# Optimization experiments

Measured on AMD Instinct MI355X. Metric: run time of the kernel, lower is better.

## Reference

```python
import jax, jax.numpy as jnp
import numpy as np

B, T, E, H, QKV = 4, 2048, 1024, 16, 64
D = E // H  # head_dim = 64


def setup_inputs() -> dict:
    key = jax.random.key(0)
    k1, k2, k3, k4 = jax.random.split(key, 4)
    scale = 1.0 / np.sqrt(D)
    x = jax.random.normal(k1, (B, T, E), dtype=jnp.float32)
    W_q = jax.random.normal(k2, (QKV, D), dtype=jnp.float32) * scale
    W_k = jax.random.normal(k3, (QKV, D), dtype=jnp.float32) * scale
    W_v = jax.random.normal(k4, (QKV, D), dtype=jnp.float32) * scale
    return {"x": x, "W_q": W_q, "W_k": W_k, "W_v": W_v}


def reference(x, W_q, W_k, W_v):
    Bx, Tx, Ex = x.shape
    d = Ex // H
    # [B,T,E] -> [B,H,T,D]  (same as torch view + permute(0,2,1,3))
    xh = x.reshape(Bx, Tx, H, d).transpose(0, 2, 1, 3)
    # Shared per-head projections: Linear(d -> qkv_dim), weight stored [out,in]
    Q = jnp.einsum("bhtd,qd->bhtq", xh, W_q)
    K = jnp.einsum("bhtd,qd->bhtq", xh, W_k)
    V = jnp.einsum("bhtd,qd->bhtq", xh, W_v)
    # NOTE: original scales by head_dim**0.5, not qkv_dim**0.5
    scores = jnp.einsum("bhtq,bhsq->bhts", Q, K) / jnp.asarray(d, x.dtype) ** 0.5
    attn = jax.nn.softmax(scores, axis=-1)
    out = jnp.einsum("bhts,bhsq->bhtq", attn, V) + V  # attention + V residual
    # per-head concat on last dim == head-major merge: [B,H,T,Q] -> [B,T,H*Q]
    return out.transpose(0, 2, 1, 3).reshape(Bx, Tx, H * W_q.shape[0])
```

## Files before the change

### kernel.cpp

```cpp
#include <hip/hip_runtime.h>

#define T_SEQ 2048
#define N_B   4
#define N_H   16
#define D_H   64
#define EMB   1024
#define CSC   0.18033688011f

typedef __attribute__((ext_vector_type(8))) short vshort8;
typedef __attribute__((ext_vector_type(4))) float vfloat4;

__device__ __forceinline__ ushort f2bf(float f) {
  union { float f; unsigned u; } v; v.f = f;
  unsigned u = v.u;
  return (ushort)((u + 0x7fffu + ((u >> 16) & 1u)) >> 16);
}
__device__ __forceinline__ unsigned pk2bf(float a, float b) {
  return (unsigned)f2bf(a) | ((unsigned)f2bf(b) << 16);
}
__device__ __forceinline__ float bf2f(ushort b) {
  union { unsigned u; float f; } v; v.u = ((unsigned)b) << 16;
  return v.f;
}
__device__ __forceinline__ float fexp2(float x) {
#if __has_builtin(__builtin_amdgcn_exp2f)
  return __builtin_amdgcn_exp2f(x);
#else
  return exp2f(x);
#endif
}
__device__ __forceinline__ unsigned permhi(float hi, float lo) {
  union { float f; unsigned u; } a, b; a.f = hi; b.f = lo;
#if __has_builtin(__builtin_amdgcn_perm)
  return __builtin_amdgcn_perm(a.u, b.u, 0x07060302u);
#else
  return (a.u & 0xFFFF0000u) | (b.u >> 16);
#endif
}


__global__ __launch_bounds__(256, 2) void proj_qkv(
    const float* __restrict__ x, const float* __restrict__ Wq,
    const float* __restrict__ Wk, const float* __restrict__ Wv,
    uint2* __restrict__ Qb, uint2* __restrict__ Kb, uint2* __restrict__ Vb) {
  const int wid  = threadIdx.x >> 6;
  const int lane = threadIdx.x & 63;
  const int l15  = lane & 15;
  const int quad = lane >> 4;
  const int gw = blockIdx.x * 4 + wid;
  const int rg = gw >> 4;
  const int h  = gw & 15;
  const int r0 = rg * 64;
  const int b  = r0 >> 11;
  const int bh = b * N_H + h;
  const int ts0 = (r0 & (T_SEQ - 1)) >> 4;

  vshort8 afr[4][2];
#pragma unroll
  for (int st = 0; st < 4; ++st) {
    const float* xp = x + (size_t)(r0 + st * 16 + l15) * EMB + h * D_H + quad * 8;
#pragma unroll
    for (int kc = 0; kc < 2; ++kc) {
      float4 a0 = *(const float4*)(xp + kc * 32);
      float4 a1 = *(const float4*)(xp + kc * 32 + 4);
      vshort8 t;
      t[0] = (short)f2bf(a0.x); t[1] = (short)f2bf(a0.y);
      t[2] = (short)f2bf(a0.z); t[3] = (short)f2bf(a0.w);
      t[4] = (short)f2bf(a1.x); t[5] = (short)f2bf(a1.y);
      t[6] = (short)f2bf(a1.z); t[7] = (short)f2bf(a1.w);
      afr[st][kc] = t;
    }
  }

  const float* Ws[3] = {Wq, Wk, Wv};
  uint2*       Bs[3] = {Qb, Kb, Vb};
#pragma unroll
  for (int m = 0; m < 3; ++m) {
    vshort8 wf[2][4];
#pragma unroll
    for (int kc = 0; kc < 2; ++kc)
#pragma unroll
      for (int nt = 0; nt < 4; ++nt) {
        const float* wp = Ws[m] + (nt * 16 + l15) * D_H + kc * 32 + quad * 8;
        float4 w0 = *(const float4*)(wp);
        float4 w1 = *(const float4*)(wp + 4);
        vshort8 t;
        t[0] = (short)f2bf(w0.x); t[1] = (short)f2bf(w0.y);
        t[2] = (short)f2bf(w0.z); t[3] = (short)f2bf(w0.w);
        t[4] = (short)f2bf(w1.x); t[5] = (short)f2bf(w1.y);
        t[6] = (short)f2bf(w1.z); t[7] = (short)f2bf(w1.w);
        wf[kc][nt] = t;
      }
    vfloat4 acc[4][4];
#pragma unroll
    for (int st = 0; st < 4; ++st)
#pragma unroll
      for (int nt = 0; nt < 4; ++nt) acc[st][nt] = (vfloat4){0.f, 0.f, 0.f, 0.f};
#pragma unroll
    for (int st = 0; st < 4; ++st)
#pragma unroll
      for (int kc = 0; kc < 2; ++kc)
#pragma unroll
        for (int nt = 0; nt < 4; ++nt)
          acc[st][nt] = (m < 2)
            ? __builtin_amdgcn_mfma_f32_16x16x32_bf16(wf[kc][nt], afr[st][kc], acc[st][nt], 0, 0, 0)
            : __builtin_amdgcn_mfma_f32_16x16x32_bf16(afr[st][kc], wf[kc][nt], acc[st][nt], 0, 0, 0);
    uint2* B = Bs[m];
#pragma unroll
    for (int st = 0; st < 4; ++st)
#pragma unroll
      for (int nt = 0; nt < 4; ++nt) {
        vfloat4 a = acc[st][nt];
        if (m == 0) { a[0] *= CSC; a[1] *= CSC; a[2] *= CSC; a[3] *= CSC; }
        uint2 w;
        w.x = pk2bf(a[0], a[1]);
        w.y = pk2bf(a[2], a[3]);
        B[(((size_t)bh * 128 + ts0 + st) * 4 + nt) * 64 + l15 * 4 + quad] = w;
      }
  }
}

__global__ __launch_bounds__(256, 2) void attn_fused(
    const uint2* __restrict__ Qb, const uint2* __restrict__ Kb,
    const uint2* __restrict__ Vb, float* __restrict__ out) {
  __shared__ ushort Pa[4 * 1024];

  const int tid  = threadIdx.x;
  const int wid  = tid >> 6;
  const int lane = tid & 63;
  const int l15  = lane & 15;
  const int quad = lane >> 4;
  const int qh   = quad >> 1;
  const int q1   = quad & 1;

  const int blk  = blockIdx.x;
  const int work = (blk & 7) * 64 + (blk >> 3);
  const int bh   = work >> 3;
  const int tblk = work & 7;
  const int b = bh >> 4, h = bh & 15;
  const int tstrip0 = tblk * 16 + wid * 4;

  const size_t hb = (size_t)bh * 128;
  const int laneoff = l15 * 4 + 2 * q1;

  vshort8 qf[4][2];
#pragma unroll
  for (int st = 0; st < 4; ++st)
#pragma unroll
    for (int kc = 0; kc < 2; ++kc)
      qf[st][kc] = *(const vshort8*)(&Qb[((hb + tstrip0 + st) * 4 + 2 * kc + qh) * 64 + laneoff]);

  vfloat4 oacc[4][4];
  float lsum[4];
#pragma unroll
  for (int st = 0; st < 4; ++st) {
#pragma unroll
    for (int nt = 0; nt < 4; ++nt) oacc[st][nt] = (vfloat4){0.f, 0.f, 0.f, 0.f};
    lsum[st] = 0.f;
  }

  ushort* Paw = &Pa[wid * 1024];
  const int parow = l15 * 64;
  const int swz   = l15 & 7;

  for (int ss = 0; ss < 128; ss += 4) {
    vshort8 kf[4][2];
#pragma unroll
    for (int snt = 0; snt < 4; ++snt)
#pragma unroll
      for (int kc = 0; kc < 2; ++kc)
        kf[snt][kc] = *(const vshort8*)(&Kb[((hb + ss + snt) * 4 + 2 * kc + qh) * 64 + laneoff]);
    vshort8 vf[2][4];
#pragma unroll
    for (int kc2 = 0; kc2 < 2; ++kc2)
#pragma unroll
      for (int dnt = 0; dnt < 4; ++dnt)
        vf[kc2][dnt] = *(const vshort8*)(&Vb[((hb + ss + 2 * kc2 + qh) * 4 + dnt) * 64 + laneoff]);

#pragma unroll
    for (int st = 0; st < 4; ++st) {
      vfloat4 sacc[4];
#pragma unroll
      for (int nt = 0; nt < 4; ++nt) sacc[nt] = (vfloat4){0.f, 0.f, 0.f, 0.f};
#pragma unroll
      for (int kc = 0; kc < 2; ++kc)
#pragma unroll
        for (int nt = 0; nt < 4; ++nt)
          sacc[nt] = __builtin_amdgcn_mfma_f32_16x16x32_bf16(kf[nt][kc], qf[st][kc], sacc[nt], 0, 0, 0);

      float ls = 0.f;
#pragma unroll
      for (int nt = 0; nt < 4; ++nt) {
        const float p0 = fexp2(sacc[nt][0]);
        const float p1 = fexp2(sacc[nt][1]);
        const float p2 = fexp2(sacc[nt][2]);
        const float p3 = fexp2(sacc[nt][3]);
        ls += (p0 + p1) + (p2 + p3);
        uint2 w;
        w.x = permhi(p1, p0);
        w.y = permhi(p3, p2);
        *(uint2*)(&Paw[parow + (((2 * nt + qh) ^ swz) << 3) + 4 * q1]) = w;
      }
      lsum[st] += ls;

#pragma unroll
      for (int kc2 = 0; kc2 < 2; ++kc2) {
        vshort8 pf = *(const vshort8*)(&Paw[parow + (((4 * kc2 + quad) ^ swz) << 3)]);
#pragma unroll
        for (int dnt = 0; dnt < 4; ++dnt)
          oacc[st][dnt] = __builtin_amdgcn_mfma_f32_16x16x32_bf16(pf, vf[kc2][dnt], oacc[st][dnt], 0, 0, 0);
      }
    }
  }

#pragma unroll
  for (int st = 0; st < 4; ++st) {
    float l = lsum[st];
    l += __shfl_xor(l, 16, 64);
    l += __shfl_xor(l, 32, 64);
    const float inv = 1.0f / l;
    float iT[4];
#pragma unroll
    for (int r = 0; r < 4; ++r) iT[r] = __shfl(inv, quad * 4 + r, 64);
    const int tstrip = tstrip0 + st;
#pragma unroll
    for (int nt = 0; nt < 4; ++nt) {
      uint2 vr = Vb[((hb + tstrip) * 4 + nt) * 64 + l15 * 4 + quad];
      float vres[4];
      vres[0] = bf2f((ushort)(vr.x & 0xFFFFu));
      vres[1] = bf2f((ushort)(vr.x >> 16));
      vres[2] = bf2f((ushort)(vr.y & 0xFFFFu));
      vres[3] = bf2f((ushort)(vr.y >> 16));
#pragma unroll
      for (int r = 0; r < 4; ++r) {
        const int t = tstrip * 16 + quad * 4 + r;
        out[((size_t)(b * T_SEQ + t)) * EMB + h * D_H + nt * 16 + l15] =
            oacc[st][nt][r] * iT[r] + vres[r];
      }
    }
  }
}

extern "C" void kernel_launch(void* const* d_in, const int* in_sizes, int n_in,
                              void* d_out, int out_size, void* d_ws, size_t ws_size,
                              hipStream_t stream) {
  const float* x  = (const float*)d_in[0];
  const float* Wq = (const float*)d_in[1];
  const float* Wk = (const float*)d_in[2];
  const float* Wv = (const float*)d_in[3];
  float* out = (float*)d_out;

  const size_t per = (size_t)64 * 128 * 4 * 16 * 4;
  uint2* Qb = (uint2*)d_ws;
  uint2* Kb = Qb + per;
  uint2* Vb = Kb + per;

  proj_qkv<<<512, 256, 0, stream>>>(x, Wq, Wk, Wv, Qb, Kb, Vb);
  attn_fused<<<512, 256, 0, stream>>>(Qb, Kb, Vb, out);
}
```

Measured before the change: 173.0 us.

## Pre-convert weights, shrink projection tiles, double-buffer K loads in attention

Adds a tiny kernel that converts the three weight matrices to bf16 MFMA fragment layout once, so the projection kernel no longer reconverts them per wave. The projection kernel now handles one 16-row strip per wave with 2048 blocks and a higher occupancy bound, trading per-wave reuse for more parallelism. The attention loop is restructured to prefetch the next K tile into a second register buffer while computing the current one, using precomputed base pointers. This raises register pressure and adds an extra kernel launch plus workspace use.

```diff
diff --git a/kernel.cpp b/kernel.cpp
--- a/kernel.cpp
+++ b/kernel.cpp
@@ -37,86 +37,86 @@
   return (a.u & 0xFFFF0000u) | (b.u >> 16);
 #endif
 }
-
-
-__global__ __launch_bounds__(256, 2) void proj_qkv(
-    const float* __restrict__ x, const float* __restrict__ Wq,
-    const float* __restrict__ Wk, const float* __restrict__ Wv,
+__device__ __forceinline__ vshort8 cvt8(const float* p) {
+  float4 w0 = *(const float4*)(p);
+  float4 w1 = *(const float4*)(p + 4);
+  vshort8 t;
+  t[0] = (short)f2bf(w0.x); t[1] = (short)f2bf(w0.y);
+  t[2] = (short)f2bf(w0.z); t[3] = (short)f2bf(w0.w);
+  t[4] = (short)f2bf(w1.x); t[5] = (short)f2bf(w1.y);
+  t[6] = (short)f2bf(w1.z); t[7] = (short)f2bf(w1.w);
+  return t;
+}
+
+
+__global__ void wconv(const float* __restrict__ Wq, const float* __restrict__ Wk,
+                      const float* __restrict__ Wv, ushort* __restrict__ Wb) {
+  const int lane = threadIdx.x & 63;
+  const int l15  = lane & 15;
+  const int quad = lane >> 4;
+  const float* Ws[3] = {Wq, Wk, Wv};
+#pragma unroll
+  for (int m = 0; m < 3; ++m)
+#pragma unroll
+    for (int kc = 0; kc < 2; ++kc)
+#pragma unroll
+      for (int nt = 0; nt < 4; ++nt) {
+        vshort8 t = cvt8(Ws[m] + (nt * 16 + l15) * D_H + kc * 32 + quad * 8);
+        *(vshort8*)(&Wb[(((m * 2 + kc) * 4 + nt) * 64 + lane) * 8]) = t;
+      }
+}
+
+__global__ __launch_bounds__(256, 4) void proj_qkv(
+    const float* __restrict__ x, const ushort* __restrict__ Wb,
     uint2* __restrict__ Qb, uint2* __restrict__ Kb, uint2* __restrict__ Vb) {
   const int wid  = threadIdx.x >> 6;
   const int lane = threadIdx.x & 63;
   const int l15  = lane & 15;
   const int quad = lane >> 4;
-  const int gw = blockIdx.x * 4 + wid;
-  const int rg = gw >> 4;
-  const int h  = gw & 15;
-  const int r0 = rg * 64;
-  const int b  = r0 >> 11;
-  const int bh = b * N_H + h;
-  const int ts0 = (r0 & (T_SEQ - 1)) >> 4;
-
-  vshort8 afr[4][2];
-#pragma unroll
-  for (int st = 0; st < 4; ++st) {
-    const float* xp = x + (size_t)(r0 + st * 16 + l15) * EMB + h * D_H + quad * 8;
-#pragma unroll
-    for (int kc = 0; kc < 2; ++kc) {
-      float4 a0 = *(const float4*)(xp + kc * 32);
-      float4 a1 = *(const float4*)(xp + kc * 32 + 4);
-      vshort8 t;
-      t[0] = (short)f2bf(a0.x); t[1] = (short)f2bf(a0.y);
-      t[2] = (short)f2bf(a0.z); t[3] = (short)f2bf(a0.w);
-      t[4] = (short)f2bf(a1.x); t[5] = (short)f2bf(a1.y);
-      t[6] = (short)f2bf(a1.z); t[7] = (short)f2bf(a1.w);
-      afr[st][kc] = t;
-    }
-  }
-
-  const float* Ws[3] = {Wq, Wk, Wv};
-  uint2*       Bs[3] = {Qb, Kb, Vb};
+  const int gw    = blockIdx.x * 4 + wid;
+  const int strip = gw >> 4;
+  const int h     = gw & 15;
+  const int r0    = strip * 16;
+  const int b     = r0 >> 11;
+  const int bh    = b * N_H + h;
+  const int ts    = (r0 & (T_SEQ - 1)) >> 4;
+
+  vshort8 afr[2];
+  {
+    const float* xp = x + (size_t)(r0 + l15) * EMB + h * D_H + quad * 8;
+    afr[0] = cvt8(xp);
+    afr[1] = cvt8(xp + 32);
+  }
+
+  uint2* Bs[3] = {Qb, Kb, Vb};
 #pragma unroll
   for (int m = 0; m < 3; ++m) {
     vshort8 wf[2][4];
 #pragma unroll
     for (int kc = 0; kc < 2; ++kc)
 #pragma unroll
-      for (int nt = 0; nt < 4; ++nt) {
-        const float* wp = Ws[m] + (nt * 16 + l15) * D_H + kc * 32 + quad * 8;
-        float4 w0 = *(const float4*)(wp);
-        float4 w1 = *(const float4*)(wp + 4);
-        vshort8 t;
-        t[0] = (short)f2bf(w0.x); t[1] = (short)f2bf(w0.y);
-        t[2] = (short)f2bf(w0.z); t[3] = (short)f2bf(w0.w);
-        t[4] = (short)f2bf(w1.x); t[5] = (short)f2bf(w1.y);
-        t[6] = (short)f2bf(w1.z); t[7] = (short)f2bf(w1.w);
-        wf[kc][nt] = t;
-      }
-    vfloat4 acc[4][4];
-#pragma unroll
-    for (int st = 0; st < 4; ++st)
-#pragma unroll
-      for (int nt = 0; nt < 4; ++nt) acc[st][nt] = (vfloat4){0.f, 0.f, 0.f, 0.f};
-#pragma unroll
-    for (int st = 0; st < 4; ++st)
-#pragma unroll
-      for (int kc = 0; kc < 2; ++kc)
-#pragma unroll
-        for (int nt = 0; nt < 4; ++nt)
-          acc[st][nt] = (m < 2)
-            ? __builtin_amdgcn_mfma_f32_16x16x32_bf16(wf[kc][nt], afr[st][kc], acc[st][nt], 0, 0, 0)
-            : __builtin_amdgcn_mfma_f32_16x16x32_bf16(afr[st][kc], wf[kc][nt], acc[st][nt], 0, 0, 0);
+      for (int nt = 0; nt < 4; ++nt)
+        wf[kc][nt] = *(const vshort8*)(&Wb[(((m * 2 + kc) * 4 + nt) * 64 + lane) * 8]);
+    vfloat4 acc[4];
+#pragma unroll
+    for (int nt = 0; nt < 4; ++nt) acc[nt] = (vfloat4){0.f, 0.f, 0.f, 0.f};
+#pragma unroll
+    for (int kc = 0; kc < 2; ++kc)
+#pragma unroll
+      for (int nt = 0; nt < 4; ++nt)
+        acc[nt] = (m < 2)
+          ? __builtin_amdgcn_mfma_f32_16x16x32_bf16(wf[kc][nt], afr[kc], acc[nt], 0, 0, 0)
+          : __builtin_amdgcn_mfma_f32_16x16x32_bf16(afr[kc], wf[kc][nt], acc[nt], 0, 0, 0);
     uint2* B = Bs[m];
 #pragma unroll
-    for (int st = 0; st < 4; ++st)
-#pragma unroll
-      for (int nt = 0; nt < 4; ++nt) {
-        vfloat4 a = acc[st][nt];
-        if (m == 0) { a[0] *= CSC; a[1] *= CSC; a[2] *= CSC; a[3] *= CSC; }
-        uint2 w;
-        w.x = pk2bf(a[0], a[1]);
-        w.y = pk2bf(a[2], a[3]);
-        B[(((size_t)bh * 128 + ts0 + st) * 4 + nt) * 64 + l15 * 4 + quad] = w;
-      }
+    for (int nt = 0; nt < 4; ++nt) {
+      vfloat4 a = acc[nt];
+      if (m == 0) { a[0] *= CSC; a[1] *= CSC; a[2] *= CSC; a[3] *= CSC; }
+      uint2 w;
+      w.x = pk2bf(a[0], a[1]);
+      w.y = pk2bf(a[2], a[3]);
+      B[(((size_t)bh * 128 + ts) * 4 + nt) * 64 + l15 * 4 + quad] = w;
+    }
   }
 }
 
@@ -143,6 +143,9 @@
   const size_t hb = (size_t)bh * 128;
   const int laneoff = l15 * 4 + 2 * q1;
 
+  const uint2* kbase = Kb + hb * 256 + qh * 64 + laneoff;
+  const uint2* vbase = Vb + hb * 256 + qh * 256 + laneoff;
+
   vshort8 qf[4][2];
 #pragma unroll
   for (int st = 0; st < 4; ++st)
@@ -163,20 +166,21 @@
   const int parow = l15 * 64;
   const int swz   = l15 & 7;
 
-  for (int ss = 0; ss < 128; ss += 4) {
-    vshort8 kf[4][2];
+  auto loadK = [&](vshort8 (&kf)[4][2], int ssb) {
 #pragma unroll
     for (int snt = 0; snt < 4; ++snt)
 #pragma unroll
       for (int kc = 0; kc < 2; ++kc)
-        kf[snt][kc] = *(const vshort8*)(&Kb[((hb + ss + snt) * 4 + 2 * kc + qh) * 64 + laneoff]);
-    vshort8 vf[2][4];
+        kf[snt][kc] = *(const vshort8*)(kbase + (ssb + snt) * 256 + kc * 128);
+  };
+  auto loadV = [&](vshort8 (&vf)[2][4], int ssb) {
 #pragma unroll
     for (int kc2 = 0; kc2 < 2; ++kc2)
 #pragma unroll
       for (int dnt = 0; dnt < 4; ++dnt)
-        vf[kc2][dnt] = *(const vshort8*)(&Vb[((hb + ss + 2 * kc2 + qh) * 4 + dnt) * 64 + laneoff]);
-
+        vf[kc2][dnt] = *(const vshort8*)(vbase + (ssb + 2 * kc2) * 256 + dnt * 64);
+  };
+  auto body = [&](vshort8 (&kf)[4][2], vshort8 (&vf)[2][4]) {
 #pragma unroll
     for (int st = 0; st < 4; ++st) {
       vfloat4 sacc[4];
@@ -211,6 +215,18 @@
           oacc[st][dnt] = __builtin_amdgcn_mfma_f32_16x16x32_bf16(pf, vf[kc2][dnt], oacc[st][dnt], 0, 0, 0);
       }
     }
+  };
+
+  vshort8 kfA[4][2], kfB[4][2], vf[2][4];
+  loadK(kfA, 0);
+#pragma unroll 1
+  for (int ss = 0; ss < 128; ss += 8) {
+    loadK(kfB, ss + 4);
+    loadV(vf, ss);
+    body(kfA, vf);
+    loadK(kfA, (ss + 8) & 127);
+    loadV(vf, ss + 4);
+    body(kfB, vf);
   }
 
 #pragma unroll
@@ -254,7 +270,9 @@
   uint2* Qb = (uint2*)d_ws;
   uint2* Kb = Qb + per;
   uint2* Vb = Kb + per;
-
-  proj_qkv<<<512, 256, 0, stream>>>(x, Wq, Wk, Wv, Qb, Kb, Vb);
+  ushort* Wb = (ushort*)(Vb + per);
+
+  wconv<<<1, 64, 0, stream>>>(Wq, Wk, Wv, Wb);
+  proj_qkv<<<2048, 256, 0, stream>>>(x, Wb, Qb, Kb, Vb);
   attn_fused<<<512, 256, 0, stream>>>(Qb, Kb, Vb, out);
 }
```

Measured after the change: 271.6 us. 57.0% more time.
